# Kernel optimization log

Hardware: AMD Instinct MI355X
Metric: run time of the kernel (lower is better)

The kernel has to match this reference:

```python
import jax, jax.numpy as jnp
import numpy as np

N_NODES = 50000
N_EDGES = 1600000
F_IN = 256
HID = 256
HEADS = 8
HD = HID // HEADS  # 32
SLOPE = 0.2
EPS = 1e-5


def setup_inputs() -> dict:
    key = jax.random.key(0)
    ks = jax.random.split(key, 10)
    node_features = jax.random.normal(ks[0], (N_NODES, F_IN), jnp.float32)
    edge_index = jax.random.randint(ks[1], (2, N_EDGES), 0, N_NODES, jnp.int32)
    s = 1.0 / np.sqrt(F_IN)
    W = jax.random.uniform(ks[2], (HEADS, F_IN, HD), jnp.float32, -s, s)
    bw = jax.random.uniform(ks[3], (HEADS, HD), jnp.float32, -s, s)
    sa = 1.0 / np.sqrt(2 * HD)
    A = jax.random.uniform(ks[4], (HEADS, 2 * HD), jnp.float32, -sa, sa)
    ba = jax.random.uniform(ks[5], (HEADS,), jnp.float32, -sa, sa)
    gamma = jnp.ones((HEADS, HD), jnp.float32)
    beta = jnp.zeros((HEADS, HD), jnp.float32)
    so = 1.0 / np.sqrt(HD)
    Wout = jax.random.uniform(ks[6], (HD, HID), jnp.float32, -so, so)
    bout = jax.random.uniform(ks[7], (HID,), jnp.float32, -so, so)
    return dict(node_features=node_features, edge_index=edge_index, W=W, bw=bw,
                A=A, ba=ba, gamma=gamma, beta=beta, Wout=Wout, bout=bout)


def _head(x, W, bw, a, ba, gamma, beta, tgt, src):
    h = x @ W + bw                         # [N, d]
    # attn(concat(h_i, h_j)) = h_i @ a1 + h_j @ a2 + ba  (linear over concat)
    si = h @ a[:HD]                        # [N]
    sj = h @ a[HD:]                        # [N]
    e = si[tgt] + sj[src] + ba             # [E]
    e = jnp.where(e >= 0, e, SLOPE * e)    # leaky_relu
    # scatter_softmax over edges grouped by target node (stable)
    m = jax.ops.segment_max(e, tgt, num_segments=N_NODES)
    ex = jnp.exp(e - m[tgt])
    den = jax.ops.segment_sum(ex, tgt, num_segments=N_NODES)
    alpha = ex / den[tgt]                  # [E]  (dropout in eval mode = identity)
    msg = alpha[:, None] * h[src]          # [E, d]
    agg = jax.ops.segment_sum(msg, tgt, num_segments=N_NODES)  # [N, d]
    out = agg + h                          # skip connection
    out = jnp.where(out > 0, out, jnp.expm1(out))  # ELU
    mu = out.mean(axis=-1, keepdims=True)
    var = out.var(axis=-1, keepdims=True)
    return (out - mu) * jax.lax.rsqrt(var + EPS) * gamma + beta


def reference(node_features, edge_index, W, bw, A, ba, gamma, beta, Wout, bout):
    tgt = edge_index[0]
    src = edge_index[1]
    heads = jax.vmap(_head, in_axes=(None, 0, 0, 0, 0, 0, 0, None, None))(
        node_features, W, bw, A, ba, gamma, beta, tgt, src)   # [H, N, d]
    mean = heads.mean(axis=0)                                  # [N, d]
    y = mean @ Wout + bout                                     # [N, HID]
    return jnp.where(y > 0, y, jnp.expm1(y))                   # ELU
```

## Files before the change

### kernel.cpp

```cpp
#include <hip/hip_runtime.h>
#include <hip/hip_bf16.h>

#define N_NODES 50000
#define N_EDGES 1600000
#define HEADS 8
#define HD 32
#define FIN 256
#define HID 256

typedef unsigned short u16;
typedef unsigned int u32;
typedef unsigned char u8;

typedef short s8v __attribute__((ext_vector_type(8)));
typedef float f4v __attribute__((ext_vector_type(4)));
typedef float f2v __attribute__((ext_vector_type(2)));

__device__ __forceinline__ float bf2f(u16 v) {
  union { u32 u; float f; } c; c.u = ((u32)v) << 16; return c.f;
}
__device__ __forceinline__ u16 f2bf(float f) {
  union { u32 u; float f; } c; c.f = f;
  u32 u = c.u;
  return (u16)((u + 0x7FFFu + ((u >> 16) & 1u)) >> 16);
}
__device__ __forceinline__ u32 pk2(float lo, float hi) {
  return (u32)f2bf(lo) | ((u32)f2bf(hi) << 16);
}

__global__ __launch_bounds__(256) void k_wprep(const float* __restrict__ W,
                                               u16* __restrict__ Wt_g) {
  int idx = blockIdx.x * 256 + threadIdx.x;
  int d4 = idx & 7;
  int hk = idx >> 3;
  int h = hk >> 8, k = hk & 255;
  float4 w = *(const float4*)&W[hk * 32 + d4 * 4];
  int colb = h * 32 + d4 * 4;
  Wt_g[(colb + 0) * 256 + k] = f2bf(w.x);
  Wt_g[(colb + 1) * 256 + k] = f2bf(w.y);
  Wt_g[(colb + 2) * 256 + k] = f2bf(w.z);
  Wt_g[(colb + 3) * 256 + k] = f2bf(w.w);
}

__global__ __launch_bounds__(256) void k_gemm(
    const float* __restrict__ X, const u16* __restrict__ Wt_g,
    const float* __restrict__ bw, const float* __restrict__ A,
    u16* __restrict__ Hb, float* __restrict__ si, float* __restrict__ sj) {
  __shared__ __align__(16) u16 Xs[128 * 40];
  __shared__ __align__(16) u16 Wt[128 * 40];

  const int t = threadIdx.x;
  const int m0 = (blockIdx.x >> 1) * 128;
  const int n0 = (blockIdx.x & 1) * 128;
  const int w = t >> 6;
  const int lane = t & 63;
  const int l15 = lane & 15;
  const int quad = lane >> 4;
  const int wm = (w >> 1) * 64;
  const int wn = (w & 1) * 64;

  f4v acc[4][4];
#pragma unroll
  for (int i = 0; i < 4; i++)
#pragma unroll
    for (int j = 0; j < 4; j++) acc[i][j] = (f4v){0.f, 0.f, 0.f, 0.f};

  const int nl = t & 127;
  const int half = t >> 7;

  for (int k0 = 0; k0 < FIN; k0 += 32) {
#pragma unroll
    for (int p = 0; p < 4; p++) {
      int row = p * 32 + (t >> 3);
      int f4 = t & 7;
      int node = m0 + row;
      float4 xv = make_float4(0.f, 0.f, 0.f, 0.f);
      if (node < N_NODES) xv = *(const float4*)&X[node * FIN + k0 + f4 * 4];
      u32* dst = (u32*)&Xs[row * 40 + f4 * 4];
      dst[0] = pk2(xv.x, xv.y);
      dst[1] = pk2(xv.z, xv.w);
    }
    {
      const u16* wp = Wt_g + (n0 + nl) * 256 + k0 + half * 16;
      *(s8v*)&Wt[nl * 40 + half * 16]     = *(const s8v*)wp;
      *(s8v*)&Wt[nl * 40 + half * 16 + 8] = *(const s8v*)(wp + 8);
    }
    __syncthreads();
    s8v af[4], bf[4];
#pragma unroll
    for (int mi = 0; mi < 4; mi++)
      af[mi] = *(const s8v*)&Xs[(wm + mi * 16 + l15) * 40 + quad * 8];
#pragma unroll
    for (int ni = 0; ni < 4; ni++)
      bf[ni] = *(const s8v*)&Wt[(wn + ni * 16 + l15) * 40 + quad * 8];
#pragma unroll
    for (int mi = 0; mi < 4; mi++)
#pragma unroll
      for (int ni = 0; ni < 4; ni++)
        acc[mi][ni] = __builtin_amdgcn_mfma_f32_16x16x32_bf16(af[mi], bf[ni], acc[mi][ni], 0, 0, 0);
    __syncthreads();
  }

  const int head0 = (n0 + wn) >> 5;
  const int head1 = head0 + 1;
  float c1a0 = A[head0 * 64 + l15],      c1a1 = A[head0 * 64 + 16 + l15];
  float c2a0 = A[head0 * 64 + 32 + l15], c2a1 = A[head0 * 64 + 48 + l15];
  float c1b0 = A[head1 * 64 + l15],      c1b1 = A[head1 * 64 + 16 + l15];
  float c2b0 = A[head1 * 64 + 32 + l15], c2b1 = A[head1 * 64 + 48 + l15];

#pragma unroll
  for (int mi = 0; mi < 4; mi++) {
#pragma unroll
    for (int ni = 0; ni < 4; ni++) {
      float b = bw[n0 + wn + ni * 16 + l15];
#pragma unroll
      for (int r = 0; r < 4; r++) acc[mi][ni][r] += b;
    }
    const int rbase = m0 + wm + mi * 16 + quad * 4;
#pragma unroll
    for (int r = 0; r < 4; r++) {
      int node = rbase + r;
      if (node < N_NODES) {
#pragma unroll
        for (int ni = 0; ni < 4; ni++) {
          int col = n0 + wn + ni * 16 + l15;
          Hb[node * HID + col] = f2bf(acc[mi][ni][r]);
        }
      }
    }
    float s1a[4], s2a[4], s1b[4], s2b[4];
#pragma unroll
    for (int r = 0; r < 4; r++) {
      s1a[r] = acc[mi][0][r] * c1a0 + acc[mi][1][r] * c1a1;
      s2a[r] = acc[mi][0][r] * c2a0 + acc[mi][1][r] * c2a1;
      s1b[r] = acc[mi][2][r] * c1b0 + acc[mi][3][r] * c1b1;
      s2b[r] = acc[mi][2][r] * c2b0 + acc[mi][3][r] * c2b1;
    }
#pragma unroll
    for (int off = 1; off <= 8; off <<= 1) {
#pragma unroll
      for (int r = 0; r < 4; r++) {
        s1a[r] += __shfl_xor(s1a[r], off);
        s2a[r] += __shfl_xor(s2a[r], off);
        s1b[r] += __shfl_xor(s1b[r], off);
        s2b[r] += __shfl_xor(s2b[r], off);
      }
    }
    if (l15 == 0) {
#pragma unroll
      for (int r = 0; r < 4; r++) {
        int node = rbase + r;
        if (node < N_NODES) {
          si[node * HEADS + head0] = s1a[r];
          sj[node * HEADS + head0] = s2a[r];
          si[node * HEADS + head1] = s1b[r];
          sj[node * HEADS + head1] = s2b[r];
        }
      }
    }
  }
}

__global__ __launch_bounds__(256) void k_cvt(const u16* __restrict__ Hb,
                                             u8* __restrict__ Hq) {
  int idx = blockIdx.x * 256 + threadIdx.x;
  const u32* p = (const u32*)Hb + (size_t)idx * 4;
  u32 w0 = p[0], w1 = p[1], w2 = p[2], w3 = p[3];
  float f0 = bf2f((u16)w0), f1 = bf2f((u16)(w0 >> 16));
  float f2 = bf2f((u16)w1), f3 = bf2f((u16)(w1 >> 16));
  float f4 = bf2f((u16)w2), f5 = bf2f((u16)(w2 >> 16));
  float f6 = bf2f((u16)w3), f7 = bf2f((u16)(w3 >> 16));
  u32 qa = __builtin_amdgcn_cvt_pk_fp8_f32(f0, f1, 0, false);
  qa = __builtin_amdgcn_cvt_pk_fp8_f32(f2, f3, qa, true);
  u32 qb = __builtin_amdgcn_cvt_pk_fp8_f32(f4, f5, 0, false);
  qb = __builtin_amdgcn_cvt_pk_fp8_f32(f6, f7, qb, true);
  u32* q = (u32*)Hq + (size_t)idx * 2;
  q[0] = qa; q[1] = qb;
}

__global__ void k_hist(const int* __restrict__ tgt, int* __restrict__ cnt) {
  int e = blockIdx.x * 256 + threadIdx.x;
  if (e < N_EDGES) atomicAdd(&cnt[tgt[e]], 1);
}

__global__ __launch_bounds__(256) void k_scan1(const int* __restrict__ cnt,
    int* __restrict__ excl, int* __restrict__ bsum) {
  __shared__ int s[256];
  const int t = threadIdx.x;
  const int i = blockIdx.x * 256 + t;
  int v = (i < N_NODES) ? cnt[i] : 0;
  s[t] = v;
  __syncthreads();
  int x = v;
  for (int off = 1; off < 256; off <<= 1) {
    int y = (t >= off) ? s[t - off] : 0;
    __syncthreads();
    x += y;
    s[t] = x;
    __syncthreads();
  }
  if (i < N_NODES) excl[i] = x - v;
  if (t == 255) bsum[blockIdx.x] = x;
}

__global__ __launch_bounds__(256) void k_scan2(const int* __restrict__ bsum,
                                               int* __restrict__ boff) {
  __shared__ int s[256];
  const int t = threadIdx.x;
  int v = (t < 196) ? bsum[t] : 0;
  s[t] = v;
  __syncthreads();
  int x = v;
  for (int off = 1; off < 256; off <<= 1) {
    int y = (t >= off) ? s[t - off] : 0;
    __syncthreads();
    x += y;
    s[t] = x;
    __syncthreads();
  }
  if (t < 196) boff[t] = x - v;
}

__global__ void k_scan3(const int* __restrict__ excl, const int* __restrict__ boff,
                        int* __restrict__ rowptr, int* __restrict__ cursor) {
  int i = blockIdx.x * 256 + threadIdx.x;
  if (i < N_NODES) {
    int v = excl[i] + boff[blockIdx.x];
    rowptr[i] = v;
    cursor[i] = v;
  }
}

__global__ void k_scatter(const int* __restrict__ tgt, const int* __restrict__ src,
                          int* __restrict__ cursor, int* __restrict__ sortedSrc) {
  int e = blockIdx.x * 256 + threadIdx.x;
  if (e < N_EDGES) {
    int tg = tgt[e];
    int pos = atomicAdd(&cursor[tg], 1);
    sortedSrc[pos] = src[e];
  }
}

__global__ __launch_bounds__(256) void k_fused(
    const u8* __restrict__ Hq, const u16* __restrict__ Hb,
    const float* __restrict__ si, const float* __restrict__ sj,
    const float* __restrict__ ba, const float* __restrict__ gamma,
    const float* __restrict__ beta, const float* __restrict__ Wout,
    const float* __restrict__ bout, const int* __restrict__ rowptr,
    const int* __restrict__ cnt, const int* __restrict__ sortedSrc,
    float* __restrict__ out) {
  __shared__ float exs[32 * 8];
  __shared__ u32   soff[32];
  __shared__ float sbase[8];
  __shared__ float accs[16][256];
  __shared__ float dens[16][16];
  __shared__ float lnorm[256];
  __shared__ float meanv[32];

  const int n = blockIdx.x;
  const int t = threadIdx.x;
  const int cg = t & 15;
  const int es = t >> 4;
  const int hh = cg >> 1;
  const int start = rowptr[n];
  const int deg = cnt[n];
  if (t < 8) sbase[t] = si[n * HEADS + t] + ba[t];
  __syncthreads();

  const int i2c = t >> 3, h8 = t & 7;
  float acc[16];
#pragma unroll
  for (int j = 0; j < 16; j++) acc[j] = 0.f;
  float den = 0.f;
  for (int base = 0; base < deg; base += 32) {
    const int m = min(32, deg - base);
    {
      float exv = 0.f;
      u32 off0 = 0;
      if (i2c < m) {
        int s = sortedSrc[start + base + i2c];
        float e = sbase[h8] + sj[s * HEADS + h8];
        e = (e >= 0.f) ? e : 0.2f * e;
        exv = __expf(e);
        off0 = (u32)s * 256u;
      }
      exs[i2c * 8 + h8] = exv;
      if (h8 == 0) soff[i2c] = off0;
    }
    __syncthreads();
#pragma unroll
    for (int k = 0; k < 2; k++) {
      int i2 = k * 16 + es;
      u32 off = soff[i2];
      float exv = exs[i2 * 8 + hh];
      float4 q4 = *(const float4*)(Hq + off + 16 * cg);
      const u32* qw = (const u32*)&q4;
#pragma unroll
      for (int d = 0; d < 4; d++) {
        f2v lo = __builtin_amdgcn_cvt_pk_f32_fp8(qw[d], false);
        f2v hi = __builtin_amdgcn_cvt_pk_f32_fp8(qw[d], true);
        acc[4 * d + 0] += exv * lo.x;
        acc[4 * d + 1] += exv * lo.y;
        acc[4 * d + 2] += exv * hi.x;
        acc[4 * d + 3] += exv * hi.y;
      }
      den += exv;
    }
    __syncthreads();
  }
#pragma unroll
  for (int j = 0; j < 16; j++)
    accs[es][cg * 16 + ((j + 2 * cg + es) & 15)] = acc[j];
  dens[es][cg] = den;
  __syncthreads();

  const int cgq = t >> 4, jq = t & 15;
  float accT = 0.f, denT = 0.f;
#pragma unroll
  for (int e2 = 0; e2 < 16; e2++) {
    accT += accs[e2][cgq * 16 + ((jq + 2 * cgq + e2) & 15)];
    denT += dens[e2][cgq];
  }
  float hs = bf2f(Hb[n * HID + t]);
  float v = ((deg > 0) ? (accT / denT) : 0.f) + hs;
  v = (v > 0.f) ? v : expm1f(v);
  float sum = v, sq = v * v;
#pragma unroll
  for (int off = 16; off >= 1; off >>= 1) {
    sum += __shfl_xor(sum, off);
    sq  += __shfl_xor(sq, off);
  }
  float mu = sum * (1.f / 32.f);
  float var = sq * (1.f / 32.f) - mu * mu;
  float nv = (v - mu) * rsqrtf(var + 1e-5f) * gamma[t] + beta[t];
  lnorm[t] = nv;
  __syncthreads();
  if (t < 32) {
    float m2 = 0.f;
#pragma unroll
    for (int h2 = 0; h2 < HEADS; h2++) m2 += lnorm[h2 * 32 + t];
    meanv[t] = m2 * 0.125f;
  }
  __syncthreads();
  float y = bout[t];
#pragma unroll
  for (int k = 0; k < 32; k++) y += meanv[k] * Wout[k * HID + t];
  y = (y > 0.f) ? y : expm1f(y);
  out[n * HID + t] = y;
}

extern "C" void kernel_launch(void* const* d_in, const int* in_sizes, int n_in,
                              void* d_out, int out_size, void* d_ws, size_t ws_size,
                              hipStream_t stream) {
  const float* X     = (const float*)d_in[0];
  const int*   EI    = (const int*)d_in[1];
  const float* W     = (const float*)d_in[2];
  const float* bw    = (const float*)d_in[3];
  const float* A     = (const float*)d_in[4];
  const float* ba    = (const float*)d_in[5];
  const float* gamma = (const float*)d_in[6];
  const float* beta  = (const float*)d_in[7];
  const float* Wout  = (const float*)d_in[8];
  const float* bout  = (const float*)d_in[9];
  float* out = (float*)d_out;
  const int* tgt = EI;
  const int* src = EI + N_EDGES;

  char* ws = (char*)d_ws;
  size_t off = 0;
  auto alloc = [&](size_t bytes) -> void* {
    void* p = ws + off;
    off += bytes;
    off = (off + 255) & ~(size_t)255;
    return p;
  };
  u16*   Hb        = (u16*)  alloc((size_t)N_NODES * HID * 2);
  u8*    Hq        = (u8*)   alloc((size_t)N_NODES * HID);
  u16*   Wt_g      = (u16*)  alloc((size_t)HID * FIN * 2);
  float* si        = (float*)alloc((size_t)N_NODES * HEADS * 4);
  float* sj        = (float*)alloc((size_t)N_NODES * HEADS * 4);
  int*   cnt       = (int*)  alloc((size_t)N_NODES * 4);
  int*   excl      = (int*)  alloc((size_t)N_NODES * 4);
  int*   bsum      = (int*)  alloc(256 * 4);
  int*   boff      = (int*)  alloc(256 * 4);
  int*   rowptr    = (int*)  alloc((size_t)N_NODES * 4);
  int*   cursor    = (int*)  alloc((size_t)N_NODES * 4);
  int*   sortedSrc = (int*)  alloc((size_t)N_EDGES * 4);

  hipMemsetAsync(cnt, 0, (size_t)N_NODES * 4, stream);
  k_hist<<<(N_EDGES + 255) / 256, 256, 0, stream>>>(tgt, cnt);
  k_scan1<<<196, 256, 0, stream>>>(cnt, excl, bsum);
  k_scan2<<<1, 256, 0, stream>>>(bsum, boff);
  k_scan3<<<196, 256, 0, stream>>>(excl, boff, rowptr, cursor);
  k_scatter<<<(N_EDGES + 255) / 256, 256, 0, stream>>>(tgt, src, cursor, sortedSrc);
  k_wprep<<<64, 256, 0, stream>>>(W, Wt_g);
  k_gemm<<<((N_NODES + 127) / 128) * 2, 256, 0, stream>>>(X, Wt_g, bw, A, Hb, si, sj);
  k_cvt<<<(N_NODES * HID / 8 + 255) / 256, 256, 0, stream>>>(Hb, Hq);
  k_fused<<<N_NODES, 256, 0, stream>>>(Hq, Hb, si, sj, ba, gamma, beta, Wout, bout,
                                       rowptr, cnt, sortedSrc, out);
}
```

Before: 540.4 us.

## Process one node per wavefront in fused GAT aggregation kernel

Restructures the fused aggregation kernel so each 64-lane wavefront handles one node, with four nodes per block, instead of one 256-thread block per node. Each lane owns four feature columns and walks the edges four at a time, computing the attention weight itself and using no shared memory or block barriers. LayerNorm, the head mean and the output projection are done with wave shuffles. Each lane now loads 4 bytes per edge instead of 16, and every lane redundantly computes exp for its head, in exchange for removing the per-32-edge syncs and the shared-memory reductions.

After: 744.9 us. 37.8% more time.

```diff
diff --git a/kernel.cpp b/kernel.cpp
--- a/kernel.cpp
+++ b/kernel.cpp
@@ -249,104 +249,95 @@
     const float* __restrict__ bout, const int* __restrict__ rowptr,
     const int* __restrict__ cnt, const int* __restrict__ sortedSrc,
     float* __restrict__ out) {
-  __shared__ float exs[32 * 8];
-  __shared__ u32   soff[32];
-  __shared__ float sbase[8];
-  __shared__ float accs[16][256];
-  __shared__ float dens[16][16];
-  __shared__ float lnorm[256];
-  __shared__ float meanv[32];
-
-  const int n = blockIdx.x;
-  const int t = threadIdx.x;
-  const int cg = t & 15;
-  const int es = t >> 4;
-  const int hh = cg >> 1;
+  const int n = blockIdx.x * 4 + (threadIdx.x >> 6);
+  if (n >= N_NODES) return;
+  const int l = threadIdx.x & 63;
+  const int h = l >> 3;
   const int start = rowptr[n];
   const int deg = cnt[n];
-  if (t < 8) sbase[t] = si[n * HEADS + t] + ba[t];
-  __syncthreads();
-
-  const int i2c = t >> 3, h8 = t & 7;
-  float acc[16];
-#pragma unroll
-  for (int j = 0; j < 16; j++) acc[j] = 0.f;
-  float den = 0.f;
-  for (int base = 0; base < deg; base += 32) {
-    const int m = min(32, deg - base);
-    {
-      float exv = 0.f;
-      u32 off0 = 0;
-      if (i2c < m) {
-        int s = sortedSrc[start + base + i2c];
-        float e = sbase[h8] + sj[s * HEADS + h8];
-        e = (e >= 0.f) ? e : 0.2f * e;
-        exv = __expf(e);
-        off0 = (u32)s * 256u;
-      }
-      exs[i2c * 8 + h8] = exv;
-      if (h8 == 0) soff[i2c] = off0;
-    }
-    __syncthreads();
-#pragma unroll
-    for (int k = 0; k < 2; k++) {
-      int i2 = k * 16 + es;
-      u32 off = soff[i2];
-      float exv = exs[i2 * 8 + hh];
-      float4 q4 = *(const float4*)(Hq + off + 16 * cg);
-      const u32* qw = (const u32*)&q4;
-#pragma unroll
-      for (int d = 0; d < 4; d++) {
-        f2v lo = __builtin_amdgcn_cvt_pk_f32_fp8(qw[d], false);
-        f2v hi = __builtin_amdgcn_cvt_pk_f32_fp8(qw[d], true);
-        acc[4 * d + 0] += exv * lo.x;
-        acc[4 * d + 1] += exv * lo.y;
-        acc[4 * d + 2] += exv * hi.x;
-        acc[4 * d + 3] += exv * hi.y;
-      }
-      den += exv;
-    }
-    __syncthreads();
-  }
-#pragma unroll
-  for (int j = 0; j < 16; j++)
-    accs[es][cg * 16 + ((j + 2 * cg + es) & 15)] = acc[j];
-  dens[es][cg] = den;
-  __syncthreads();
-
-  const int cgq = t >> 4, jq = t & 15;
-  float accT = 0.f, denT = 0.f;
-#pragma unroll
-  for (int e2 = 0; e2 < 16; e2++) {
-    accT += accs[e2][cgq * 16 + ((jq + 2 * cgq + e2) & 15)];
-    denT += dens[e2][cgq];
-  }
-  float hs = bf2f(Hb[n * HID + t]);
-  float v = ((deg > 0) ? (accT / denT) : 0.f) + hs;
-  v = (v > 0.f) ? v : expm1f(v);
-  float sum = v, sq = v * v;
-#pragma unroll
-  for (int off = 16; off >= 1; off >>= 1) {
+  const float sb = si[n * HEADS + h] + ba[h];
+
+  float a0 = 0.f, a1 = 0.f, a2 = 0.f, a3 = 0.f, den = 0.f;
+  for (int i = 0; i < deg; i += 4) {
+    int sidx[4];
+#pragma unroll
+    for (int k = 0; k < 4; k++)
+      sidx[k] = (i + k < deg) ? sortedSrc[start + i + k] : -1;
+    float ex[4];
+    u32 q[4];
+#pragma unroll
+    for (int k = 0; k < 4; k++) {
+      int s = (sidx[k] >= 0) ? sidx[k] : 0;
+      float e = sb + sj[s * HEADS + h];
+      e = (e >= 0.f) ? e : 0.2f * e;
+      ex[k] = (sidx[k] >= 0) ? __expf(e) : 0.f;
+      q[k] = *(const u32*)(Hq + (size_t)s * 256 + 4 * l);
+    }
+#pragma unroll
+    for (int k = 0; k < 4; k++) {
+      f2v lo = __builtin_amdgcn_cvt_pk_f32_fp8(q[k], false);
+      f2v hi = __builtin_amdgcn_cvt_pk_f32_fp8(q[k], true);
+      a0 += ex[k] * lo.x;
+      a1 += ex[k] * lo.y;
+      a2 += ex[k] * hi.x;
+      a3 += ex[k] * hi.y;
+      den += ex[k];
+    }
+  }
+  const float inv = (deg > 0) ? 1.f / den : 0.f;
+
+  const u32* hp = (const u32*)(Hb + (size_t)n * HID + 4 * l);
+  u32 h01 = hp[0], h23 = hp[1];
+  float v0 = a0 * inv + bf2f((u16)h01);
+  float v1 = a1 * inv + bf2f((u16)(h01 >> 16));
+  float v2 = a2 * inv + bf2f((u16)h23);
+  float v3 = a3 * inv + bf2f((u16)(h23 >> 16));
+  v0 = (v0 > 0.f) ? v0 : expm1f(v0);
+  v1 = (v1 > 0.f) ? v1 : expm1f(v1);
+  v2 = (v2 > 0.f) ? v2 : expm1f(v2);
+  v3 = (v3 > 0.f) ? v3 : expm1f(v3);
+
+  float sum = v0 + v1 + v2 + v3;
+  float sq = v0 * v0 + v1 * v1 + v2 * v2 + v3 * v3;
+#pragma unroll
+  for (int off = 1; off <= 4; off <<= 1) {
     sum += __shfl_xor(sum, off);
     sq  += __shfl_xor(sq, off);
   }
   float mu = sum * (1.f / 32.f);
   float var = sq * (1.f / 32.f) - mu * mu;
-  float nv = (v - mu) * rsqrtf(var + 1e-5f) * gamma[t] + beta[t];
-  lnorm[t] = nv;
-  __syncthreads();
-  if (t < 32) {
-    float m2 = 0.f;
-#pragma unroll
-    for (int h2 = 0; h2 < HEADS; h2++) m2 += lnorm[h2 * 32 + t];
-    meanv[t] = m2 * 0.125f;
-  }
-  __syncthreads();
-  float y = bout[t];
-#pragma unroll
-  for (int k = 0; k < 32; k++) y += meanv[k] * Wout[k * HID + t];
-  y = (y > 0.f) ? y : expm1f(y);
-  out[n * HID + t] = y;
+  float rs = rsqrtf(var + 1e-5f);
+  float4 gm = *(const float4*)&gamma[4 * l];
+  float4 bt = *(const float4*)&beta[4 * l];
+  float m0 = (v0 - mu) * rs * gm.x + bt.x;
+  float m1 = (v1 - mu) * rs * gm.y + bt.y;
+  float m2 = (v2 - mu) * rs * gm.z + bt.z;
+  float m3 = (v3 - mu) * rs * gm.w + bt.w;
+
+#pragma unroll
+  for (int off = 8; off <= 32; off <<= 1) {
+    m0 += __shfl_xor(m0, off);
+    m1 += __shfl_xor(m1, off);
+    m2 += __shfl_xor(m2, off);
+    m3 += __shfl_xor(m3, off);
+  }
+  float mv[4] = {m0 * 0.125f, m1 * 0.125f, m2 * 0.125f, m3 * 0.125f};
+
+  float4 y = *(const float4*)&bout[4 * l];
+#pragma unroll
+  for (int k = 0; k < 32; k++) {
+    float mk = __shfl(mv[k & 3], k >> 2);
+    float4 wv = *(const float4*)&Wout[k * HID + 4 * l];
+    y.x += mk * wv.x;
+    y.y += mk * wv.y;
+    y.z += mk * wv.z;
+    y.w += mk * wv.w;
+  }
+  y.x = (y.x > 0.f) ? y.x : expm1f(y.x);
+  y.y = (y.y > 0.f) ? y.y : expm1f(y.y);
+  y.z = (y.z > 0.f) ? y.z : expm1f(y.z);
+  y.w = (y.w > 0.f) ? y.w : expm1f(y.w);
+  *(float4*)&out[(size_t)n * HID + 4 * l] = y;
 }
 
 extern "C" void kernel_launch(void* const* d_in, const int* in_sizes, int n_in,
@@ -396,6 +387,6 @@
   k_wprep<<<64, 256, 0, stream>>>(W, Wt_g);
   k_gemm<<<((N_NODES + 127) / 128) * 2, 256, 0, stream>>>(X, Wt_g, bw, A, Hb, si, sj);
   k_cvt<<<(N_NODES * HID / 8 + 255) / 256, 256, 0, stream>>>(Hb, Hq);
-  k_fused<<<N_NODES, 256, 0, stream>>>(Hq, Hb, si, sj, ba, gamma, beta, Wout, bout,
-                                       rowptr, cnt, sortedSrc, out);
-}
+  k_fused<<<(N_NODES + 3) / 4, 256, 0, stream>>>(Hq, Hb, si, sj, ba, gamma, beta,
+                                                 Wout, bout, rowptr, cnt, sortedSrc, out);
+}
```
